# Performance work log

Hardware: AMD Instinct MI355X
Metric: run time of the kernel (lower is better)

## Reference

```python
import jax, jax.numpy as jnp
import numpy as np

TEMPERATURE = 1.0
STRIDE = 1
PADDING = 2
RF = 5  # receptive_field_size
TREE_DEPTH = 3

# Each of the 16 binary difflogic ops op_g(a,b) is multilinear:
# op_g = c0 + c1*a + c2*b + c3*a*b. Rows ordered per the standard difflogic table:
# 0:0, 1:a&b, 2:a&~b, 3:a, 4:~a&b, 5:b, 6:xor, 7:or, 8:nor, 9:xnor,
# 10:~b, 11:a|~b, 12:~a, 13:~a|b, 14:nand, 15:1
_C = jnp.asarray(np.array([
    [0, 0, 0, 0],
    [0, 0, 0, 1],
    [0, 1, 0, -1],
    [0, 1, 0, 0],
    [0, 0, 1, -1],
    [0, 0, 1, 0],
    [0, 1, 1, -2],
    [0, 1, 1, -1],
    [1, -1, -1, 1],
    [1, -1, -1, 2],
    [1, 0, -1, 0],
    [1, 0, -1, 1],
    [1, -1, 0, 0],
    [1, -1, 0, 1],
    [1, 0, 0, -1],
    [1, 0, 0, 0]], dtype=np.float32))


def _gate(a, b, logits):
    """Soft LUT gate. a,b: (B,K,N,P); logits: (N,K,16) -> (B,K,N,P)."""
    w = jax.nn.softmax(logits / TEMPERATURE, axis=-1)          # (N,K,16)
    coef = jnp.einsum('nkg,gc->knc', w, _C)                    # (K,N,4)
    c = coef[None, :, :, None, :]                              # (1,K,N,1,4)
    return c[..., 0] + c[..., 1] * a + c[..., 2] * b + c[..., 3] * (a * b)


def setup_inputs() -> dict:
    key = jax.random.key(0)
    ks = jax.random.split(key, 8)
    B, Cin, H, W = 16, 32, 64, 64
    K, N = 64, 2 ** TREE_DEPTH  # num_kernels, leaf gates per tree
    x = jax.random.uniform(ks[0], (B, Cin, H, W), dtype=jnp.float32)
    idx_h = jax.random.randint(ks[1], (2, K, N), 0, RF, dtype=jnp.int32)
    idx_w = jax.random.randint(ks[2], (2, K, N), 0, RF, dtype=jnp.int32)
    idx_c = jax.random.randint(ks[3], (2, K, N), 0, Cin, dtype=jnp.int32)
    w0 = jax.random.normal(ks[4], (8, K, 16), dtype=jnp.float32)
    w1 = jax.random.normal(ks[5], (4, K, 16), dtype=jnp.float32)
    w2 = jax.random.normal(ks[6], (2, K, 16), dtype=jnp.float32)
    w3 = jax.random.normal(ks[7], (1, K, 16), dtype=jnp.float32)
    return {"x": x, "idx_h": idx_h, "idx_w": idx_w, "idx_c": idx_c,
            "w0": w0, "w1": w1, "w2": w2, "w3": w3}


def reference(x, idx_h, idx_w, idx_c, w0, w1, w2, w3):
    B, Cin, H, W = x.shape
    xp = jnp.pad(x, ((0, 0), (0, 0), (PADDING, PADDING), (PADDING, PADDING)))
    out_h = (H + 2 * PADDING - RF) // STRIDE + 1
    out_w = (W + 2 * PADDING - RF) // STRIDE + 1
    # Absolute gather coords per (rank-slot, kernel, leaf-gate, out_y, out_x)
    abs_h = idx_h[..., None, None] + (jnp.arange(out_h) * STRIDE)[:, None]   # (2,K,N,oh,1)
    abs_w = idx_w[..., None, None] + (jnp.arange(out_w) * STRIDE)[None, :]   # (2,K,N,1,ow)
    cc = idx_c[..., None, None]                                              # (2,K,N,1,1)
    g = xp[:, cc, abs_h, abs_w]                                # (B,2,K,N,oh,ow)
    K, N = g.shape[2], g.shape[3]
    g = g.reshape(B, 2, K, N, out_h * out_w)                   # (B,2,K,N,P)
    cur = _gate(g[:, 0], g[:, 1], w0)                          # (B,K,8,P) leaf level
    for wl in (w1, w2, w3):                                    # reduce tree: 8->4->2->1
        cur = _gate(cur[:, :, 0::2, :], cur[:, :, 1::2, :], wl)
    return cur.reshape(B, K, out_h, out_w)
```

## Files before the change

kernel.cpp:

```cpp
#include <hip/hip_runtime.h>
#include <hip/hip_bf16.h>

#define CIN 32
#define HW 64
#define KK 64
#define NLEAF 8
#define PADDING 2
#define PW 68
#define PIMG (PW * PW)
#define NPADBLK 2312

typedef float f32x4 __attribute__((ext_vector_type(4)));

__device__ __constant__ float d_C[16][4] = {
    {0, 0, 0, 0},  {0, 0, 0, 1},  {0, 1, 0, -1}, {0, 1, 0, 0},
    {0, 0, 1, -1}, {0, 0, 1, 0},  {0, 1, 1, -2}, {0, 1, 1, -1},
    {1, -1, -1, 1},{1, -1, -1, 2},{1, 0, -1, 0}, {1, 0, -1, 1},
    {1, -1, 0, 0}, {1, -1, 0, 1}, {1, 0, 0, -1}, {1, 0, 0, 0}
};

__global__ __launch_bounds__(256) void prep_kernel(
    const float* __restrict__ x,
    const int* __restrict__ idx_h, const int* __restrict__ idx_w, const int* __restrict__ idx_c,
    const float* __restrict__ w0, const float* __restrict__ w1,
    const float* __restrict__ w2, const float* __restrict__ w3,
    float* __restrict__ coefA, int* __restrict__ loffA, float* __restrict__ xpad)
{
    int blk = blockIdx.x;
    if (blk < NPADBLK) {
        int t = blk * 256 + threadIdx.x;
        #pragma unroll
        for (int it = 0; it < 4; ++it) {
            int e  = t + it * (NPADBLK * 256);
            int bc = e / PIMG;
            int r  = e - bc * PIMG;
            int ph = r / PW;
            int pw = r - ph * PW;
            int ih = ph - PADDING, iw = pw - PADDING;
            float v = 0.f;
            if ((unsigned)ih < HW && (unsigned)iw < HW)
                v = x[bc * (HW * HW) + ih * HW + iw];
            xpad[e] = v;
        }
        return;
    }
    int t = (blk - NPADBLK) * 256 + threadIdx.x;

    {
        int k = t >> 4, n = t & 15;
        int s = n >> 3, leaf = n & 7;
        int o = s * (KK * NLEAF) + k * NLEAF + leaf;
        loffA[t] = idx_c[o] * PIMG + idx_h[o] * PW + idx_w[o];
    }

    if (t < KK * 15) {
        int k = t / 15, node = t % 15;
        const float* wp; int n;
        if (node < 8)       { wp = w0; n = node; }
        else if (node < 12) { wp = w1; n = node - 8; }
        else if (node < 14) { wp = w2; n = node - 12; }
        else                { wp = w3; n = 0; }
        const float4* lp = (const float4*)(wp + (size_t)(n * KK + k) * 16);
        float4 L0 = lp[0], L1 = lp[1], L2 = lp[2], L3 = lp[3];
        float l[16] = {L0.x, L0.y, L0.z, L0.w, L1.x, L1.y, L1.z, L1.w,
                       L2.x, L2.y, L2.z, L2.w, L3.x, L3.y, L3.z, L3.w};
        float m = l[0];
        #pragma unroll
        for (int g = 1; g < 16; ++g) m = fmaxf(m, l[g]);
        float p[16], s = 0.f;
        #pragma unroll
        for (int g = 0; g < 16; ++g) { p[g] = __expf(l[g] - m); s += p[g]; }
        float inv = 1.f / s;
        float c0 = 0, c1 = 0, c2 = 0, c3 = 0;
        #pragma unroll
        for (int g = 0; g < 16; ++g) {
            float w = p[g] * inv;
            c0 = fmaf(w, d_C[g][0], c0);
            c1 = fmaf(w, d_C[g][1], c1);
            c2 = fmaf(w, d_C[g][2], c2);
            c3 = fmaf(w, d_C[g][3], c3);
        }
        float* o = coefA + (k * 60 + node * 4);
        o[0] = c0; o[1] = c1; o[2] = c2; o[3] = c3;
    }
}

__device__ __forceinline__ f32x4 bc4(float s) { return (f32x4){s, s, s, s}; }
__device__ __forceinline__ f32x4 gate4(const float* c, f32x4 a, f32x4 b) {
    return __builtin_elementwise_fma(b,
               __builtin_elementwise_fma(a, bc4(c[3]), bc4(c[2])),
               __builtin_elementwise_fma(a, bc4(c[1]), bc4(c[0])));
}

__global__ __launch_bounds__(256) void logic_conv_kernel(
    const float* __restrict__ xpad, const int* __restrict__ loffA,
    const float* __restrict__ coefA, float* __restrict__ out)
{
    int blk = blockIdx.x;
    int b = blk & 15, k = blk >> 4;

    const float* xpb = xpad + (size_t)b * (CIN * PIMG);

    const float* bp[16];
    #pragma unroll
    for (int n = 0; n < 16; ++n)
        bp[n] = xpb + __builtin_amdgcn_readfirstlane(loffA[(k << 4) + n]);

    float cf[15][4];
    #pragma unroll
    for (int nd = 0; nd < 15; ++nd) {
        f32x4 c4 = ((const f32x4*)(coefA + k * 60))[nd];
        cf[nd][0] = c4.x; cf[nd][1] = c4.y; cf[nd][2] = c4.z; cf[nd][3] = c4.w;
    }

    float* outp = out + ((size_t)(b * KK + k) << 12);
    int p0 = threadIdx.x << 2;

    #pragma unroll
    for (int it = 0; it < 4; ++it) {
        int p    = p0 + it * 1024;
        int voff = (p >> 6) * PW + (p & 63);

        f32x4 g[16];
        #pragma unroll
        for (int n = 0; n < 16; ++n)
            g[n] = *(const f32x4*)(bp[n] + voff);

        f32x4 v[8];
        #pragma unroll
        for (int n = 0; n < 8; ++n)
            v[n] = gate4(cf[n], g[n], g[8 + n]);
        f32x4 u[4];
        #pragma unroll
        for (int n = 0; n < 4; ++n)
            u[n] = gate4(cf[8 + n], v[2 * n], v[2 * n + 1]);
        f32x4 t0 = gate4(cf[12], u[0], u[1]);
        f32x4 t1 = gate4(cf[13], u[2], u[3]);
        f32x4 r  = gate4(cf[14], t0, t1);

        __builtin_nontemporal_store(r, (f32x4*)(outp + p));
    }
}

extern "C" void kernel_launch(void* const* d_in, const int* in_sizes, int n_in,
                              void* d_out, int out_size, void* d_ws, size_t ws_size,
                              hipStream_t stream) {
    const float* x     = (const float*)d_in[0];
    const int*   idx_h = (const int*)d_in[1];
    const int*   idx_w = (const int*)d_in[2];
    const int*   idx_c = (const int*)d_in[3];
    const float* w0    = (const float*)d_in[4];
    const float* w1    = (const float*)d_in[5];
    const float* w2    = (const float*)d_in[6];
    const float* w3    = (const float*)d_in[7];
    float* out = (float*)d_out;

    float* coefA = (float*)d_ws;
    int*   loffA = (int*)((char*)d_ws + 16384);
    float* xpad  = (float*)((char*)d_ws + 32768);

    hipLaunchKernelGGL(prep_kernel, dim3(NPADBLK + 4), dim3(256), 0, stream,
                       x, idx_h, idx_w, idx_c, w0, w1, w2, w3, coefA, loffA, xpad);
    hipLaunchKernelGGL(logic_conv_kernel, dim3(1024), dim3(256), 0, stream,
                       xpad, loffA, coefA, out);
}
```

Measured before the change: 24.24 us.

## Interleave four batches per pixel and stage input tiles in LDS

```diff
diff --git a/kernel.cpp b/kernel.cpp
--- a/kernel.cpp
+++ b/kernel.cpp
@@ -6,10 +6,17 @@
 #define KK 64
 #define NLEAF 8
 #define PADDING 2
+#define TH 4
+#define TCW 16
+#define WR 8
+#define WC 20
+#define WPOS (CIN * WR * WC)
 #define PW 68
 #define PIMG (PW * PW)
-#define NPADBLK 2312
-
+#define NP4 (4 * CIN * PIMG)
+#define NPADBLK 578
+
+typedef float f32x2 __attribute__((ext_vector_type(2)));
 typedef float f32x4 __attribute__((ext_vector_type(4)));
 
 __device__ __constant__ float d_C[16][4] = {
@@ -24,33 +31,46 @@
     const int* __restrict__ idx_h, const int* __restrict__ idx_w, const int* __restrict__ idx_c,
     const float* __restrict__ w0, const float* __restrict__ w1,
     const float* __restrict__ w2, const float* __restrict__ w3,
-    float* __restrict__ coefA, int* __restrict__ loffA, float* __restrict__ xpad)
+    float* __restrict__ coefA, int* __restrict__ loffL, int* __restrict__ loffG,
+    f32x4* __restrict__ xpad4)
 {
     int blk = blockIdx.x;
     if (blk < NPADBLK) {
         int t = blk * 256 + threadIdx.x;
         #pragma unroll
         for (int it = 0; it < 4; ++it) {
-            int e  = t + it * (NPADBLK * 256);
-            int bc = e / PIMG;
-            int r  = e - bc * PIMG;
-            int ph = r / PW;
-            int pw = r - ph * PW;
-            int ih = ph - PADDING, iw = pw - PADDING;
-            float v = 0.f;
-            if ((unsigned)ih < HW && (unsigned)iw < HW)
-                v = x[bc * (HW * HW) + ih * HW + iw];
-            xpad[e] = v;
+            int e = t + it * (NPADBLK * 256);
+            if (e < NP4) {
+                int qc = e / PIMG;
+                int r  = e - qc * PIMG;
+                int q  = qc >> 5, c = qc & 31;
+                int ph = r / PW;
+                int pw = r - ph * PW;
+                int ih = ph - PADDING, iw = pw - PADDING;
+                f32x4 v = {0.f, 0.f, 0.f, 0.f};
+                if ((unsigned)ih < HW && (unsigned)iw < HW) {
+                    const float* xb = x + ((size_t)(4 * q) * CIN + c) * (HW * HW)
+                                    + ih * HW + iw;
+                    v.x = xb[0];
+                    v.y = xb[CIN * HW * HW];
+                    v.z = xb[2 * CIN * HW * HW];
+                    v.w = xb[3 * CIN * HW * HW];
+                }
+                xpad4[e] = v;
+            }
         }
         return;
     }
     int t = (blk - NPADBLK) * 256 + threadIdx.x;
 
     {
-        int k = t >> 4, n = t & 15;
-        int s = n >> 3, leaf = n & 7;
-        int o = s * (KK * NLEAF) + k * NLEAF + leaf;
-        loffA[t] = idx_c[o] * PIMG + idx_h[o] * PW + idx_w[o];
+        int side = t >> 9, r = t & 511;
+        int k = r >> 3, leaf = r & 7;
+        int o = side * (KK * NLEAF) + k * NLEAF + leaf;
+        if (side == 0)
+            loffL[r] = (idx_c[o] * (WR * WC) + idx_h[o] * WC + idx_w[o]) * 16;
+        else
+            loffG[r] = idx_c[o] * PIMG + idx_h[o] * PW + idx_w[o];
     }
 
     if (t < KK * 15) {
@@ -92,53 +112,79 @@
                __builtin_elementwise_fma(a, bc4(c[1]), bc4(c[0])));
 }
 
-__global__ __launch_bounds__(256) void logic_conv_kernel(
-    const float* __restrict__ xpad, const int* __restrict__ loffA,
-    const float* __restrict__ coefA, float* __restrict__ out)
+__global__ __launch_bounds__(512, 4) void logic_conv_kernel(
+    const f32x4* __restrict__ xpad4, const int* __restrict__ loffL,
+    const int* __restrict__ loffG, const float* __restrict__ coefA,
+    float* __restrict__ out)
 {
-    int blk = blockIdx.x;
-    int b = blk & 15, k = blk >> 4;
-
-    const float* xpb = xpad + (size_t)b * (CIN * PIMG);
-
-    const float* bp[16];
+    extern __shared__ f32x4 xt[];
+
+    int tid  = threadIdx.x;
+    int grp  = blockIdx.x & 7;
+    int quad = grp & 3;
+    int kh   = grp >> 2;
+    int t    = blockIdx.x >> 3;
+    int r0   = (t >> 2) * TH;
+    int c0   = (t & 3) * TCW;
+
+    const f32x4* xq = xpad4 + (size_t)quad * (CIN * PIMG);
+
     #pragma unroll
-    for (int n = 0; n < 16; ++n)
-        bp[n] = xpb + __builtin_amdgcn_readfirstlane(loffA[(k << 4) + n]);
-
-    float cf[15][4];
-    #pragma unroll
-    for (int nd = 0; nd < 15; ++nd) {
-        f32x4 c4 = ((const f32x4*)(coefA + k * 60))[nd];
-        cf[nd][0] = c4.x; cf[nd][1] = c4.y; cf[nd][2] = c4.z; cf[nd][3] = c4.w;
-    }
-
-    float* outp = out + ((size_t)(b * KK + k) << 12);
-    int p0 = threadIdx.x << 2;
-
-    #pragma unroll
-    for (int it = 0; it < 4; ++it) {
-        int p    = p0 + it * 1024;
-        int voff = (p >> 6) * PW + (p & 63);
-
-        f32x4 g[16];
-        #pragma unroll
-        for (int n = 0; n < 16; ++n)
-            g[n] = *(const f32x4*)(bp[n] + voff);
+    for (int i = 0; i < 10; ++i) {
+        int e  = tid + i * 512;
+        int c  = e / (WR * WC);
+        int r  = e - c * (WR * WC);
+        int rr = r / WC;
+        int cc = r - rr * WC;
+        xt[e] = xq[c * PIMG + (r0 + rr) * PW + (c0 + cc)];
+    }
+    __syncthreads();
+
+    int lane = tid & 63, wave = tid >> 6;
+    int tr = lane >> 4, tc = lane & 15;
+    int pxb   = (tr * WC + tc) * 16;
+    int voff  = (r0 + tr) * PW + (c0 + tc);
+    int pxout = (r0 + tr) * HW + (c0 + tc);
+    float* outB0 = out + ((size_t)(4 * quad) << 18);
+    float* outB1 = outB0 + (1 << 18);
+    float* outB2 = outB1 + (1 << 18);
+    float* outB3 = outB2 + (1 << 18);
+    const char* xtb = (const char*)xt;
+
+    int kbase = __builtin_amdgcn_readfirstlane(kh * 32 + wave * 4);
+
+    #pragma unroll 2
+    for (int j = 0; j < 4; ++j) {
+        int k = kbase + j;
+        const int*   LL = loffL + (k << 3);
+        const int*   LG = loffG + (k << 3);
+        const float* C  = coefA + k * 60;
+
+        f32x4 ga[8], gb[8];
+        #pragma unroll
+        for (int n = 0; n < 8; ++n)
+            gb[n] = xq[LG[n] + voff];
+        #pragma unroll
+        for (int n = 0; n < 8; ++n)
+            ga[n] = *(const f32x4*)(xtb + (LL[n] + pxb));
 
         f32x4 v[8];
         #pragma unroll
         for (int n = 0; n < 8; ++n)
-            v[n] = gate4(cf[n], g[n], g[8 + n]);
+            v[n] = gate4(C + 4 * n, ga[n], gb[n]);
         f32x4 u[4];
         #pragma unroll
         for (int n = 0; n < 4; ++n)
-            u[n] = gate4(cf[8 + n], v[2 * n], v[2 * n + 1]);
-        f32x4 t0 = gate4(cf[12], u[0], u[1]);
-        f32x4 t1 = gate4(cf[13], u[2], u[3]);
-        f32x4 r  = gate4(cf[14], t0, t1);
-
-        __builtin_nontemporal_store(r, (f32x4*)(outp + p));
+            u[n] = gate4(C + 32 + 4 * n, v[2 * n], v[2 * n + 1]);
+        f32x4 t0 = gate4(C + 48, u[0], u[1]);
+        f32x4 t1 = gate4(C + 52, u[2], u[3]);
+        f32x4 r  = gate4(C + 56, t0, t1);
+
+        int ko = (k << 12) + pxout;
+        __builtin_nontemporal_store(r.x, &outB0[ko]);
+        __builtin_nontemporal_store(r.y, &outB1[ko]);
+        __builtin_nontemporal_store(r.z, &outB2[ko]);
+        __builtin_nontemporal_store(r.w, &outB3[ko]);
     }
 }
 
@@ -156,11 +202,14 @@
     float* out = (float*)d_out;
 
     float* coefA = (float*)d_ws;
-    int*   loffA = (int*)((char*)d_ws + 16384);
-    float* xpad  = (float*)((char*)d_ws + 32768);
+    int*   loffL = (int*)((char*)d_ws + 16384);
+    int*   loffG = (int*)((char*)d_ws + 20480);
+    f32x4* xpad4 = (f32x4*)((char*)d_ws + 32768);
 
     hipLaunchKernelGGL(prep_kernel, dim3(NPADBLK + 4), dim3(256), 0, stream,
-                       x, idx_h, idx_w, idx_c, w0, w1, w2, w3, coefA, loffA, xpad);
-    hipLaunchKernelGGL(logic_conv_kernel, dim3(1024), dim3(256), 0, stream,
-                       xpad, loffA, coefA, out);
-}
+                       x, idx_h, idx_w, idx_c, w0, w1, w2, w3,
+                       coefA, loffL, loffG, xpad4);
+    hipLaunchKernelGGL(logic_conv_kernel, dim3(512), dim3(512),
+                       WPOS * sizeof(f32x4), stream,
+                       xpad4, loffL, loffG, coefA, out);
+}
```

Result: slower. 25.51 us (+5.2%).
